# Performance work log

Measured on AMD Instinct MI355X. Metric: run time of the kernel, lower is better.

Reference implementation:

```python
import jax, jax.numpy as jnp
import numpy as np

N_NODES = 100000

def _norm_coeffs(edge_index, n_nodes):
    # PyG GCNConv default: add self-loops, symmetric normalization D^-1/2 A D^-1/2
    src = jnp.concatenate([edge_index[0], jnp.arange(n_nodes, dtype=edge_index.dtype)])
    dst = jnp.concatenate([edge_index[1], jnp.arange(n_nodes, dtype=edge_index.dtype)])
    deg = jax.ops.segment_sum(jnp.ones_like(dst, dtype=jnp.float32), dst, num_segments=n_nodes)
    dinv = jnp.where(deg > 0, jax.lax.rsqrt(deg), 0.0)
    norm = dinv[src] * dinv[dst]  # [E + N]
    return src, dst, norm

def _gcn_conv(x, W, b, src, dst, norm, n_nodes):
    h = x @ W                       # [N, out] dense transform first (PyG order)
    msg = h[src] * norm[:, None]    # gather + scale, [E+N, out]
    out = jax.ops.segment_sum(msg, dst, num_segments=n_nodes)  # scatter-add aggregate
    return out + b

def setup_inputs() -> dict:
    key = jax.random.key(0)
    ks = jax.random.split(key, 8)
    in_feats, h_feats, num_classes = 128, 128, 64
    n_edges = 1_600_000
    x = jax.random.normal(ks[0], (N_NODES, in_feats), dtype=jnp.float32)
    edge_index = jax.random.randint(ks[1], (2, n_edges), 0, N_NODES, dtype=jnp.int64)
    def glorot(k, fi, fo):
        s = jnp.sqrt(6.0 / (fi + fo))
        return jax.random.uniform(k, (fi, fo), jnp.float32, -s, s)
    return {
        "x": x,
        "edge_index": edge_index,
        "W0": glorot(ks[2], in_feats, h_feats), "b0": jnp.zeros((h_feats,), jnp.float32),
        "W1": glorot(ks[3], h_feats, h_feats), "b1": jnp.zeros((h_feats,), jnp.float32),
        "W2": glorot(ks[4], h_feats, num_classes), "b2": jnp.zeros((num_classes,), jnp.float32),
    }

def reference(x, edge_index, W0, b0, W1, b1, W2, b2):
    n_nodes = x.shape[0]
    src, dst, norm = _norm_coeffs(edge_index, n_nodes)
    # layer 0 + 1: ReLU between (dropout is identity in eval mode)
    h = jax.nn.relu(_gcn_conv(x, W0, b0, src, dst, norm, n_nodes))
    h = jax.nn.relu(_gcn_conv(h, W1, b1, src, dst, norm, n_nodes))
    # final layer: no activation
    return _gcn_conv(h, W2, b2, src, dst, norm, n_nodes)
```

## Files before the change

### kernel.cpp

```cpp
#include <hip/hip_runtime.h>
#include <hip/hip_bf16.h>
#include <stdint.h>


typedef __attribute__((ext_vector_type(8))) short bf16x8;
typedef __attribute__((ext_vector_type(4))) float f32x4;

__device__ __forceinline__ float bflo(uint32_t u) { return __uint_as_float(u << 16); }
__device__ __forceinline__ float bfhi(uint32_t u) { return __uint_as_float(u & 0xffff0000u); }
__device__ __forceinline__ unsigned short f2bf(float f) {
    uint32_t x = __float_as_uint(f);
    return (unsigned short)((x + 0x7fffu + ((x >> 16) & 1u)) >> 16);
}

#define CE   4096
#define BINW 256

__global__ __launch_bounds__(256) void k_binhist(const int* __restrict__ dst,
                                                 int* __restrict__ cnt,
                                                 int NBIN, int E) {
    extern __shared__ int h[];
    int c = blockIdx.x, base = c * CE;
    for (int i = threadIdx.x; i < NBIN; i += 256) h[i] = 0;
    __syncthreads();
    for (int i = 0; i < CE; i += 256) {
        int e = base + i + threadIdx.x;
        if (e < E) atomicAdd(&h[dst[e] >> 8], 1);
    }
    __syncthreads();
    for (int i = threadIdx.x; i < NBIN; i += 256) cnt[c * NBIN + i] = h[i];
}

__global__ __launch_bounds__(256) void k_colscan(const int* __restrict__ cnt,
                                                 int* __restrict__ off_cb,
                                                 int* __restrict__ tot,
                                                 int NBIN, int NCHUNK) {
    __shared__ int part[256];
    int b = blockIdx.x, t = threadIdx.x;
    int K = (NCHUNK + 255) >> 8;
    int c0 = t * K;
    int vals[16];
    int s = 0;
    for (int k = 0; k < K; ++k) {
        int c = c0 + k;
        int v = (c < NCHUNK) ? cnt[c * NBIN + b] : 0;
        vals[k] = s;
        s += v;
    }
    part[t] = s;
    __syncthreads();
    for (int off = 1; off < 256; off <<= 1) {
        int x = (t >= off) ? part[t - off] : 0;
        __syncthreads();
        part[t] += x;
        __syncthreads();
    }
    int run = (t == 0) ? 0 : part[t - 1];
    for (int k = 0; k < K; ++k) {
        int c = c0 + k;
        if (c < NCHUNK) off_cb[c * NBIN + b] = run + vals[k];
    }
    if (t == 255) tot[b] = part[255];
}

__global__ __launch_bounds__(512) void k_binoff(const int* __restrict__ tot,
                                                int* __restrict__ bin_off,
                                                int* __restrict__ row_ptr,
                                                unsigned short* __restrict__ hzero,
                                                int NBIN, int N, int E) {
    __shared__ int part[512];
    int t = threadIdx.x;
    int v = (t < NBIN) ? tot[t] : 0;
    part[t] = v;
    __syncthreads();
    for (int off = 1; off < 512; off <<= 1) {
        int x = (t >= off) ? part[t - off] : 0;
        __syncthreads();
        part[t] += x;
        __syncthreads();
    }
    if (t < NBIN) bin_off[t] = part[t] - v;
    if (t == 0) { bin_off[NBIN] = E; row_ptr[N] = E; }
    if (t < 16) { uint4 z; z.x = z.y = z.z = z.w = 0; ((uint4*)hzero)[t] = z; }
}

__global__ __launch_bounds__(256) void k_binscatter(const int* __restrict__ src,
                                                    const int* __restrict__ dst,
                                                    const int* __restrict__ off_cb,
                                                    const int* __restrict__ bin_off,
                                                    unsigned int* __restrict__ bpack,
                                                    int NBIN, int E) {
    extern __shared__ int lcur[];
    int c = blockIdx.x, base = c * CE;
    for (int i = threadIdx.x; i < NBIN; i += 256)
        lcur[i] = off_cb[c * NBIN + i] + bin_off[i];
    __syncthreads();
    for (int i = 0; i < CE; i += 256) {
        int e = base + i + threadIdx.x;
        if (e < E) {
            int d = dst[e], s = src[e];
            int pos = atomicAdd(&lcur[d >> 8], 1);
            bpack[pos] = (unsigned)s | ((unsigned)(d & 255) << 24);
        }
    }
}

__global__ __launch_bounds__(256) void k_bindeg(const unsigned int* __restrict__ bpack,
                                                const int* __restrict__ bin_off,
                                                int* __restrict__ row_ptr,
                                                float* __restrict__ dinv, int N) {
    __shared__ int h[256];
    __shared__ int part[256];
    int b = blockIdx.x, t = threadIdx.x;
    int lo = b * BINW;
    h[t] = 0;
    __syncthreads();
    int s0 = bin_off[b], s1 = bin_off[b + 1];
    for (int i = s0 + t; i < s1; i += 256)
        atomicAdd(&h[bpack[i] >> 24], 1);
    __syncthreads();
    int dg = h[t];
    part[t] = dg;
    __syncthreads();
    for (int off = 1; off < 256; off <<= 1) {
        int x = (t >= off) ? part[t - off] : 0;
        __syncthreads();
        part[t] += x;
        __syncthreads();
    }
    if (lo + t < N) {
        row_ptr[lo + t] = s0 + part[t] - dg;
        dinv[lo + t] = rsqrtf((float)(dg + 1));
    }
}

__global__ __launch_bounds__(256) void k_csr(const unsigned int* __restrict__ bpack,
                                             const int* __restrict__ bin_off,
                                             const int* __restrict__ row_ptr,
                                             int* __restrict__ col_idx, int N) {
    __shared__ int lcur[256];
    int b = blockIdx.x, t = threadIdx.x;
    int lo = b * BINW;
    lcur[t] = (lo + t < N) ? row_ptr[lo + t] : 0;
    __syncthreads();
    int s0 = bin_off[b], s1 = bin_off[b + 1];
    for (int i = s0 + t; i < s1; i += 256) {
        unsigned pk = bpack[i];
        int pos = atomicAdd(&lcur[pk >> 24], 1);
        col_idx[pos] = (int)(pk & 0xFFFFFFu);
    }
}

__global__ __launch_bounds__(256) void k_prepw(const float* __restrict__ W0,
                                               const float* __restrict__ W1,
                                               const float* __restrict__ W2,
                                               unsigned short* __restrict__ wt0,
                                               unsigned short* __restrict__ wt1,
                                               unsigned short* __restrict__ wt2) {
    int id = blockIdx.x * 256 + threadIdx.x;
    const float* Wsrc;
    unsigned short* dst;
    int t, M, plane;
    if (id < 16384)      { t = id;         Wsrc = W0; dst = wt0; M = 128; plane = 16384; }
    else if (id < 32768) { t = id - 16384; Wsrc = W1; dst = wt1; M = 128; plane = 16384; }
    else if (id < 40960) { t = id - 32768; Wsrc = W2; dst = wt2; M = 64;  plane = 8192;  }
    else return;
    int k = (M == 128) ? (t >> 7) : (t >> 6);
    int c = (M == 128) ? (t & 127) : (t & 63);
    float v = Wsrc[k * M + c];
    unsigned short hi = f2bf(v);
    float lov = v - bflo((uint32_t)hi);
    dst[c * 128 + k]         = hi;
    dst[plane + c * 128 + k] = f2bf(lov);
}

template <int NCOL, bool BF16A>
__global__ __launch_bounds__(256) void k_gemm_mfma(
    const void* __restrict__ Av, const unsigned short* __restrict__ Wt,
    const float* __restrict__ dinv, unsigned short* __restrict__ H, int N) {
    constexpr int K = 128, KT = 64;
    constexpr int A_SH = 128 * KT;
    constexpr int APL = BF16A ? 1 : 2;
    constexpr int W_PLANE = NCOL * KT;
    __shared__ __align__(16) unsigned short sm[APL * A_SH + 2 * W_PLANE];
    unsigned short* Ah  = sm;
    unsigned short* Al  = sm + A_SH;
    unsigned short* Whp = sm + APL * A_SH;
    unsigned short* Wlp = sm + APL * A_SH + W_PLANE;

    const int tid = threadIdx.x;
    const long r0 = (long)blockIdx.x * 128;
    const int w = tid >> 6, l = tid & 63;
    const int lr = l & 15, lk = l >> 4;
    constexpr int WR = (NCOL == 128) ? 4 : 2;
    const int wrow = (NCOL == 128) ? (w >> 1) * 64 : w * 32;
    const int wcol = (NCOL == 128) ? (w & 1) * 64 : 0;

    f32x4 acc[WR][4];
#pragma unroll
    for (int i = 0; i < WR; ++i)
#pragma unroll
        for (int j = 0; j < 4; ++j) acc[i][j] = (f32x4){0.f, 0.f, 0.f, 0.f};

    for (int kt = 0; kt < 2; ++kt) {
        if (kt) __syncthreads();
#pragma unroll
        for (int it = 0; it < 4; ++it) {
            int id = it * 256 + tid;
            int r = id >> 3, kc = id & 7;
            long gr = r0 + r;
            if (gr >= N) gr = N - 1;
            int boff = r * 128 + ((kc * 16) ^ ((r & 7) << 4));
            if constexpr (BF16A) {
                const unsigned short* ap =
                    (const unsigned short*)Av + gr * K + kt * KT + kc * 8;
                *(bf16x8*)((char*)Ah + boff) = *(const bf16x8*)ap;
            } else {
                const float* ap = (const float*)Av + gr * K + kt * KT + kc * 8;
                float4 v0 = *(const float4*)ap;
                float4 v1 = *(const float4*)(ap + 4);
                float vv[8] = {v0.x, v0.y, v0.z, v0.w, v1.x, v1.y, v1.z, v1.w};
                union { unsigned short u[8]; bf16x8 v; } ph, pl;
#pragma unroll
                for (int j = 0; j < 8; ++j) {
                    unsigned short h = f2bf(vv[j]);
                    ph.u[j] = h;
                    pl.u[j] = f2bf(vv[j] - bflo((uint32_t)h));
                }
                *(bf16x8*)((char*)Ah + boff) = ph.v;
                *(bf16x8*)((char*)Al + boff) = pl.v;
            }
        }
#pragma unroll
        for (int it = 0; it < NCOL / 32; ++it) {
            int id = it * 256 + tid;
            int c = id >> 3, kc = id & 7;
            const unsigned short* wp = &Wt[c * K + kt * KT + kc * 8];
            bf16x8 vh = *(const bf16x8*)wp;
            bf16x8 vl = *(const bf16x8*)(wp + NCOL * K);
            int boff = c * 128 + ((kc * 16) ^ ((c & 7) << 4));
            *(bf16x8*)((char*)Whp + boff) = vh;
            *(bf16x8*)((char*)Wlp + boff) = vl;
        }
        __syncthreads();
#pragma unroll
        for (int ks = 0; ks < 2; ++ks) {
            int kb = ks * 64 + lk * 16;
            bf16x8 bh[4], bl[4];
#pragma unroll
            for (int cf = 0; cf < 4; ++cf) {
                int c = wcol + cf * 16 + lr;
                int off = c * 128 + (kb ^ ((c & 7) << 4));
                bh[cf] = *(bf16x8*)((char*)Whp + off);
                bl[cf] = *(bf16x8*)((char*)Wlp + off);
            }
#pragma unroll
            for (int rf = 0; rf < WR; ++rf) {
                int r = wrow + rf * 16 + lr;
                int off = r * 128 + (kb ^ ((r & 7) << 4));
                bf16x8 ah = *(bf16x8*)((char*)Ah + off);
                if constexpr (BF16A) {
#pragma unroll
                    for (int cf = 0; cf < 4; ++cf) {
                        acc[rf][cf] = __builtin_amdgcn_mfma_f32_16x16x32_bf16(ah, bh[cf], acc[rf][cf], 0, 0, 0);
                        acc[rf][cf] = __builtin_amdgcn_mfma_f32_16x16x32_bf16(ah, bl[cf], acc[rf][cf], 0, 0, 0);
                    }
                } else {
                    bf16x8 al = *(bf16x8*)((char*)Al + off);
#pragma unroll
                    for (int cf = 0; cf < 4; ++cf) {
                        acc[rf][cf] = __builtin_amdgcn_mfma_f32_16x16x32_bf16(ah, bh[cf], acc[rf][cf], 0, 0, 0);
                        acc[rf][cf] = __builtin_amdgcn_mfma_f32_16x16x32_bf16(al, bh[cf], acc[rf][cf], 0, 0, 0);
                        acc[rf][cf] = __builtin_amdgcn_mfma_f32_16x16x32_bf16(ah, bl[cf], acc[rf][cf], 0, 0, 0);
                    }
                }
            }
        }
    }
#pragma unroll
    for (int rf = 0; rf < WR; ++rf) {
        long rb = r0 + wrow + rf * 16 + lk * 4;
#pragma unroll
        for (int reg = 0; reg < 4; ++reg) {
            long r = rb + reg;
            if (r < N) {
                float dv = dinv[r];
#pragma unroll
                for (int cf = 0; cf < 4; ++cf) {
                    int c = wcol + cf * 16 + lr;
                    H[r * NCOL + c] = f2bf(dv * acc[rf][cf][reg]);
                }
            }
        }
    }
}

template <int F, bool RELU, bool OUTBF16>
__global__ __launch_bounds__(256) void k_agg(const unsigned short* __restrict__ H,
                                             const int* __restrict__ row_ptr,
                                             const int* __restrict__ col_idx,
                                             const float* __restrict__ dinv,
                                             const float* __restrict__ bias,
                                             void* __restrict__ Yv, int N) {
    constexpr int LPR = F / 8;
    constexpr int EPW = 64 / LPR;
    int lane = threadIdx.x & 63;
    int node = blockIdx.x * 4 + (threadIdx.x >> 6);
    if (node >= N) return;
    const int q  = lane / LPR;
    const int ql = lane % LPR;
    const int DUMMY = (F == 128) ? N : 2 * N;

    float acc[8];
#pragma unroll
    for (int f = 0; f < 8; ++f) acc[f] = 0.f;
    if (q == 0) {
        uint4 u = *((const uint4*)(H + (size_t)node * F) + ql);
        acc[0] = bflo(u.x); acc[1] = bfhi(u.x);
        acc[2] = bflo(u.y); acc[3] = bfhi(u.y);
        acc[4] = bflo(u.z); acc[5] = bfhi(u.z);
        acc[6] = bflo(u.w); acc[7] = bfhi(u.w);
    }

#define ACC8(u)                                                         \
    acc[0] += bflo(u.x); acc[1] += bfhi(u.x);                           \
    acc[2] += bflo(u.y); acc[3] += bfhi(u.y);                           \
    acc[4] += bflo(u.z); acc[5] += bfhi(u.z);                           \
    acc[6] += bflo(u.w); acc[7] += bfhi(u.w);

    int start = row_ptr[node], end = row_ptr[node + 1];
    for (int base = start; base < end; base += 64) {
        int idx = DUMMY;
        if (base + lane < end) idx = col_idx[base + lane];
        int cnt = min(64, end - base);
        int j = 0;
        for (; j + 4 * EPW <= cnt; j += 4 * EPW) {
            int s0 = __shfl(idx, j + q);
            int s1 = __shfl(idx, j + EPW + q);
            int s2 = __shfl(idx, j + 2 * EPW + q);
            int s3 = __shfl(idx, j + 3 * EPW + q);
            uint4 u0 = *((const uint4*)(H + (size_t)s0 * F) + ql);
            uint4 u1 = *((const uint4*)(H + (size_t)s1 * F) + ql);
            uint4 u2 = *((const uint4*)(H + (size_t)s2 * F) + ql);
            uint4 u3 = *((const uint4*)(H + (size_t)s3 * F) + ql);
            ACC8(u0); ACC8(u1); ACC8(u2); ACC8(u3);
        }
        if (j + 2 * EPW <= cnt) {
            int s0 = __shfl(idx, j + q);
            int s1 = __shfl(idx, j + EPW + q);
            uint4 u0 = *((const uint4*)(H + (size_t)s0 * F) + ql);
            uint4 u1 = *((const uint4*)(H + (size_t)s1 * F) + ql);
            ACC8(u0); ACC8(u1);
            j += 2 * EPW;
        }
        for (; j < cnt; j += EPW) {
            int s = __shfl(idx, j + q);
            uint4 u = *((const uint4*)(H + (size_t)s * F) + ql);
            ACC8(u);
        }
    }
#undef ACC8

#pragma unroll
    for (int f = 0; f < 8; ++f) {
        if constexpr (F == 64) acc[f] += __shfl_xor(acc[f], 8);
        acc[f] += __shfl_xor(acc[f], 16);
        acc[f] += __shfl_xor(acc[f], 32);
    }

    float dv = dinv[node];
    if constexpr (OUTBF16) {
        if (q == 0) {
            float4 b0 = *(const float4*)&bias[ql * 8];
            float4 b1 = *(const float4*)&bias[ql * 8 + 4];
            float y[8];
            y[0] = dv * acc[0] + b0.x; y[1] = dv * acc[1] + b0.y;
            y[2] = dv * acc[2] + b0.z; y[3] = dv * acc[3] + b0.w;
            y[4] = dv * acc[4] + b1.x; y[5] = dv * acc[5] + b1.y;
            y[6] = dv * acc[6] + b1.z; y[7] = dv * acc[7] + b1.w;
            uint4 o;
            unsigned* ow = (unsigned*)&o;
#pragma unroll
            for (int k = 0; k < 4; ++k) {
                float a0 = y[2 * k], a1 = y[2 * k + 1];
                if (RELU) { a0 = fmaxf(a0, 0.f); a1 = fmaxf(a1, 0.f); }
                ow[k] = (unsigned)f2bf(a0) | ((unsigned)f2bf(a1) << 16);
            }
            *((uint4*)((unsigned short*)Yv + (size_t)node * F) + ql) = o;
        }
    } else {
        if (q < 2) {
            int fb = ql * 8 + q * 4;
            float4 b = *(const float4*)&bias[fb];
            float4 o;
            o.x = dv * acc[q * 4 + 0] + b.x;
            o.y = dv * acc[q * 4 + 1] + b.y;
            o.z = dv * acc[q * 4 + 2] + b.z;
            o.w = dv * acc[q * 4 + 3] + b.w;
            if (RELU) {
                o.x = fmaxf(o.x, 0.f); o.y = fmaxf(o.y, 0.f);
                o.z = fmaxf(o.z, 0.f); o.w = fmaxf(o.w, 0.f);
            }
            *(float4*)((float*)Yv + (size_t)node * F + fb) = o;
        }
    }
}

extern "C" void kernel_launch(void* const* d_in, const int* in_sizes, int n_in,
                              void* d_out, int out_size, void* d_ws, size_t ws_size,
                              hipStream_t stream) {
    const float* x  = (const float*)d_in[0];
    const int* eidx = (const int*)d_in[1];
    const float* W0 = (const float*)d_in[2];
    const float* b0 = (const float*)d_in[3];
    const float* W1 = (const float*)d_in[4];
    const float* b1 = (const float*)d_in[5];
    const float* W2 = (const float*)d_in[6];
    const float* b2 = (const float*)d_in[7];
    float* out = (float*)d_out;

    const int N = in_sizes[0] / 128;
    const int E = in_sizes[1] / 2;
    const int* srcp = eidx;
    const int* dstp = eidx + E;

    const int NBIN   = (N + BINW - 1) / BINW;
    const int NCHUNK = (E + CE - 1) / CE;

    char* p = (char*)d_ws;
    auto take = [&](size_t bytes) {
        char* r = p;
        p += (bytes + 255) & ~(size_t)255;
        return r;
    };
    int*            cnt     = (int*)take((size_t)NCHUNK * NBIN * 4);
    int*            off_cb  = (int*)take((size_t)NCHUNK * NBIN * 4);
    int*            tot     = (int*)take((size_t)NBIN * 4);
    int*            bin_off = (int*)take((size_t)(NBIN + 1) * 4);
    unsigned int*   bpack   = (unsigned int*)take((size_t)E * 4);
    int*            row_ptr = (int*)take((size_t)(N + 1) * 4);
    float*          dinv    = (float*)take((size_t)N * 4);
    int*            col_idx = (int*)take((size_t)E * 4);
    unsigned short* hbuf    = (unsigned short*)take((size_t)(N + 1) * 128 * 2);
    unsigned short* ybuf    = (unsigned short*)take((size_t)N * 128 * 2);
    unsigned short* wt0     = (unsigned short*)take((size_t)2 * 16384 * 2);
    unsigned short* wt1     = (unsigned short*)take((size_t)2 * 16384 * 2);
    unsigned short* wt2     = (unsigned short*)take((size_t)2 * 8192 * 2);

    k_binhist<<<NCHUNK, 256, NBIN * 4, stream>>>(dstp, cnt, NBIN, E);
    k_prepw<<<160, 256, 0, stream>>>(W0, W1, W2, wt0, wt1, wt2);
    k_colscan<<<NBIN, 256, 0, stream>>>(cnt, off_cb, tot, NBIN, NCHUNK);
    k_binoff<<<1, 512, 0, stream>>>(tot, bin_off, row_ptr,
                                    hbuf + (size_t)N * 128, NBIN, N, E);
    k_binscatter<<<NCHUNK, 256, NBIN * 4, stream>>>(srcp, dstp, off_cb, bin_off,
                                                    bpack, NBIN, E);
    k_bindeg<<<NBIN, 256, 0, stream>>>(bpack, bin_off, row_ptr, dinv, N);
    k_csr<<<NBIN, 256, 0, stream>>>(bpack, bin_off, row_ptr, col_idx, N);

    int gemm_grid = (N + 127) / 128;
    int agg_grid  = (N + 3) / 4;

    k_gemm_mfma<128, false><<<gemm_grid, 256, 0, stream>>>(x, wt0, dinv, hbuf, N);
    k_agg<128, true, true><<<agg_grid, 256, 0, stream>>>(hbuf, row_ptr, col_idx,
                                                         dinv, b0, ybuf, N);
    k_gemm_mfma<128, true><<<gemm_grid, 256, 0, stream>>>(ybuf, wt1, dinv, hbuf, N);
    k_agg<128, true, true><<<agg_grid, 256, 0, stream>>>(hbuf, row_ptr, col_idx,
                                                         dinv, b1, ybuf, N);
    k_gemm_mfma<64, true><<<gemm_grid, 256, 0, stream>>>(ybuf, wt2, dinv, hbuf, N);
    k_agg<64, false, false><<<agg_grid, 256, 0, stream>>>(hbuf, row_ptr, col_idx,
                                                          dinv, b2, out, N);
}
```

Measured before the change: 366.9 us.

## Fuse degree and CSR kernels, truncate bf16 split, use 32-bit gather offsets

Merges the per-bin degree/row_ptr kernel and the CSR fill kernel into one launch, so bpack is read in the same block and row starts stay in shared memory. The fp32-to-bf16 hi/lo split in the GEMM A-load now truncates instead of rounding to nearest even, which saves ALU work but may change the residual split slightly. The aggregation gather computes addresses with 32-bit shifts instead of 64-bit multiplies, which assumes the feature buffer stays under 4 GB.

```diff
diff --git a/kernel.cpp b/kernel.cpp
--- a/kernel.cpp
+++ b/kernel.cpp
@@ -105,12 +105,14 @@
     }
 }
 
-__global__ __launch_bounds__(256) void k_bindeg(const unsigned int* __restrict__ bpack,
+__global__ __launch_bounds__(256) void k_bincsr(const unsigned int* __restrict__ bpack,
                                                 const int* __restrict__ bin_off,
                                                 int* __restrict__ row_ptr,
-                                                float* __restrict__ dinv, int N) {
+                                                float* __restrict__ dinv,
+                                                int* __restrict__ col_idx, int N) {
     __shared__ int h[256];
     __shared__ int part[256];
+    __shared__ int lcur[256];
     int b = blockIdx.x, t = threadIdx.x;
     int lo = b * BINW;
     h[t] = 0;
@@ -128,22 +130,13 @@
         part[t] += x;
         __syncthreads();
     }
+    int rstart = s0 + part[t] - dg;
+    lcur[t] = rstart;
     if (lo + t < N) {
-        row_ptr[lo + t] = s0 + part[t] - dg;
+        row_ptr[lo + t] = rstart;
         dinv[lo + t] = rsqrtf((float)(dg + 1));
     }
-}
-
-__global__ __launch_bounds__(256) void k_csr(const unsigned int* __restrict__ bpack,
-                                             const int* __restrict__ bin_off,
-                                             const int* __restrict__ row_ptr,
-                                             int* __restrict__ col_idx, int N) {
-    __shared__ int lcur[256];
-    int b = blockIdx.x, t = threadIdx.x;
-    int lo = b * BINW;
-    lcur[t] = (lo + t < N) ? row_ptr[lo + t] : 0;
-    __syncthreads();
-    int s0 = bin_off[b], s1 = bin_off[b + 1];
+    __syncthreads();
     for (int i = s0 + t; i < s1; i += 256) {
         unsigned pk = bpack[i];
         int pos = atomicAdd(&lcur[pk >> 24], 1);
@@ -223,9 +216,10 @@
                 union { unsigned short u[8]; bf16x8 v; } ph, pl;
 #pragma unroll
                 for (int j = 0; j < 8; ++j) {
-                    unsigned short h = f2bf(vv[j]);
-                    ph.u[j] = h;
-                    pl.u[j] = f2bf(vv[j] - bflo((uint32_t)h));
+                    uint32_t vb = __float_as_uint(vv[j]);
+                    ph.u[j] = (unsigned short)(vb >> 16);
+                    float rem = vv[j] - bfhi(vb);
+                    pl.u[j] = (unsigned short)(__float_as_uint(rem) >> 16);
                 }
                 *(bf16x8*)((char*)Ah + boff) = ph.v;
                 *(bf16x8*)((char*)Al + boff) = pl.v;
@@ -304,24 +298,28 @@
                                              void* __restrict__ Yv, int N) {
     constexpr int LPR = F / 8;
     constexpr int EPW = 64 / LPR;
+    constexpr int SH  = (F == 128) ? 8 : 7;
     int lane = threadIdx.x & 63;
     int node = blockIdx.x * 4 + (threadIdx.x >> 6);
     if (node >= N) return;
     const int q  = lane / LPR;
+    const unsigned qb = (unsigned)(lane % LPR) * 16u;
     const int ql = lane % LPR;
     const int DUMMY = (F == 128) ? N : 2 * N;
+    const char* Hb = (const char*)H;
 
     float acc[8];
 #pragma unroll
     for (int f = 0; f < 8; ++f) acc[f] = 0.f;
     if (q == 0) {
-        uint4 u = *((const uint4*)(H + (size_t)node * F) + ql);
+        uint4 u = *(const uint4*)(Hb + (((unsigned)node << SH) + qb));
         acc[0] = bflo(u.x); acc[1] = bfhi(u.x);
         acc[2] = bflo(u.y); acc[3] = bfhi(u.y);
         acc[4] = bflo(u.z); acc[5] = bfhi(u.z);
         acc[6] = bflo(u.w); acc[7] = bfhi(u.w);
     }
 
+#define GLD(s) (*(const uint4*)(Hb + (((unsigned)(s) << SH) + qb)))
 #define ACC8(u)                                                         \
     acc[0] += bflo(u.x); acc[1] += bfhi(u.x);                           \
     acc[2] += bflo(u.y); acc[3] += bfhi(u.y);                           \
@@ -339,27 +337,28 @@
             int s1 = __shfl(idx, j + EPW + q);
             int s2 = __shfl(idx, j + 2 * EPW + q);
             int s3 = __shfl(idx, j + 3 * EPW + q);
-            uint4 u0 = *((const uint4*)(H + (size_t)s0 * F) + ql);
-            uint4 u1 = *((const uint4*)(H + (size_t)s1 * F) + ql);
-            uint4 u2 = *((const uint4*)(H + (size_t)s2 * F) + ql);
-            uint4 u3 = *((const uint4*)(H + (size_t)s3 * F) + ql);
+            uint4 u0 = GLD(s0);
+            uint4 u1 = GLD(s1);
+            uint4 u2 = GLD(s2);
+            uint4 u3 = GLD(s3);
             ACC8(u0); ACC8(u1); ACC8(u2); ACC8(u3);
         }
         if (j + 2 * EPW <= cnt) {
             int s0 = __shfl(idx, j + q);
             int s1 = __shfl(idx, j + EPW + q);
-            uint4 u0 = *((const uint4*)(H + (size_t)s0 * F) + ql);
-            uint4 u1 = *((const uint4*)(H + (size_t)s1 * F) + ql);
+            uint4 u0 = GLD(s0);
+            uint4 u1 = GLD(s1);
             ACC8(u0); ACC8(u1);
             j += 2 * EPW;
         }
         for (; j < cnt; j += EPW) {
             int s = __shfl(idx, j + q);
-            uint4 u = *((const uint4*)(H + (size_t)s * F) + ql);
+            uint4 u = GLD(s);
             ACC8(u);
         }
     }
 #undef ACC8
+#undef GLD
 
 #pragma unroll
     for (int f = 0; f < 8; ++f) {
@@ -454,8 +453,8 @@
                                     hbuf + (size_t)N * 128, NBIN, N, E);
     k_binscatter<<<NCHUNK, 256, NBIN * 4, stream>>>(srcp, dstp, off_cb, bin_off,
                                                     bpack, NBIN, E);
-    k_bindeg<<<NBIN, 256, 0, stream>>>(bpack, bin_off, row_ptr, dinv, N);
-    k_csr<<<NBIN, 256, 0, stream>>>(bpack, bin_off, row_ptr, col_idx, N);
+    k_bincsr<<<NBIN, 256, 0, stream>>>(bpack, bin_off, row_ptr, dinv,
+                                       col_idx, N);
 
     int gemm_grid = (N + 127) / 128;
     int agg_grid  = (N + 3) / 4;
```

Measured after the change: 371.6 us. About the same (+1.3%).
